# Kernel optimization log

Hardware: AMD Instinct MI355X
Metric: run time of the kernel (lower is better)

Reference implementation:

```python
import jax, jax.numpy as jnp
import numpy as np


def setup_inputs() -> dict:
    B, S, D, V = 2, 4096, 512, 32000
    FE_START, FE_LEN = 5, 3062          # user-controllable span [5, 3067)
    ADV_START, ADV_LEN = 1000, 64       # adversarial suffix block
    ML = ADV_START - FE_START           # 995 = max_left_shift
    MR = FE_LEN - (ADV_START - FE_START + ADV_LEN)  # 2003 = max_right_shift
    key = jax.random.key(0)
    k1, k2 = jax.random.split(key)
    input_ids = jax.random.randint(k1, (B, S), 0, V, dtype=jnp.int32)
    suffix_mask = jnp.zeros((B, S), dtype=bool).at[:, ADV_START:ADV_START + ADV_LEN].set(True)
    # param initialized like _create_parameters: delta at index max_left_shift
    param = jnp.zeros((1, ML + MR + 1), dtype=jnp.float32).at[0, ML].set(1.0)
    emb_weight = jax.random.normal(k2, (V, D), dtype=jnp.float32) * 0.02
    return {
        'input_ids': input_ids, 'suffix_mask': suffix_mask,
        'param': param, 'emb_weight': emb_weight,
        'fe_start': FE_START, 'fe_len': FE_LEN, 'adv_len': ADV_LEN,
        'max_left_shift': ML, 'max_right_shift': MR,
    }


def _padded_kernel(param, ml, mr):
    left_pad = max(0, mr - ml)
    right_pad = max(0, ml - mr)
    # F.pad then flip, as in torch forward
    return jnp.flip(jnp.pad(param, ((0, 0), (left_pad, right_pad)))[0])  # (Kp,)


def reference(input_ids, suffix_mask, param, emb_weight,
              fe_start, fe_len, adv_len, max_left_shift, max_right_shift):
    B, S = input_ids.shape
    D = emb_weight.shape[1]
    Kp = 2 * max(max_left_shift, max_right_shift) + 1
    p = Kp // 2  # 'same' padding
    pk = _padded_kernel(param, max_left_shift, max_right_shift).astype(emb_weight.dtype)

    embeds = emb_weight[input_ids]                       # (B,S,D)
    fe = embeds[:, fe_start:fe_start + fe_len]           # frontend-user gather (contiguous)
    fe_pad = jnp.pad(fe, ((0, 0), (p, p), (0, 0)))       # (B, F+2p, D)
    # depthwise conv1d with a single shared kernel == Toeplitz matmul
    off = jnp.arange(fe_len + 2 * p)[None, :] - jnp.arange(fe_len)[:, None]
    W = jnp.where((off >= 0) & (off < Kp), pk[jnp.clip(off, 0, Kp - 1)], 0.0)  # (F, F+2p)
    new_fe = jnp.einsum('tu,bud->btd', W, fe_pad)        # (B,F,D)
    # scatter-concat: other[:extra0] | shifted user span | other[extra1:]
    out_embeds = jnp.concatenate(
        [embeds[:, :fe_start], new_fe, embeds[:, fe_start + fe_len:]], axis=1)

    # ----- id path (no_grad in original) -----
    L = adv_len
    ms = p - jnp.argmax(pk == 1.0)                       # mask_shift
    a0 = jnp.argmax(suffix_mask, axis=-1)                # (B,) current_start
    ns = a0 + ms                                         # new_start
    idx = jnp.arange(S - L)[None, :]
    src = idx + L * (idx >= a0[:, None])                 # skip the adv block
    nonadv = jnp.take_along_axis(input_ids, src, axis=1)             # (B,S-L)
    adv = jnp.take_along_axis(input_ids, a0[:, None] + jnp.arange(L)[None, :], axis=1)
    j = jnp.arange(S)[None, :]
    in_adv = (j >= ns[:, None]) & (j < ns[:, None] + L)
    idx_non = jnp.clip(jnp.where(j < ns[:, None], j, j - L), 0, S - L - 1)
    idx_adv = jnp.clip(j - ns[:, None], 0, L - 1)
    out_ids = jnp.where(in_adv,
                        jnp.take_along_axis(adv, idx_adv, axis=1),
                        jnp.take_along_axis(nonadv, idx_non, axis=1))
    return out_embeds, out_ids
```

## Files before the change

kernel.cpp:

```cpp
#include <hip/hip_runtime.h>
#include <limits.h>

#define BB 2
#define SS 4096
#define DD 512
#define VV 32000
#define FE_START 5
#define FE_LEN 3062
#define ADV_LEN 64
#define ML 995
#define MR 2003
#define KP (2 * MR + 1)
#define PHALF (KP / 2)
#define LEFT_PAD (MR - ML)
#define PARAM_LEN (ML + MR + 1)


__global__ void ABS_meta_kernel(const unsigned char* __restrict__ mask_bytes,
                                const float* __restrict__ param,
                                int* __restrict__ meta,
                                int tap_cap) {
    __shared__ int s_nnz;
    __shared__ int s_msi;
    __shared__ int s_first;
    __shared__ int s_layout;
    __shared__ int s_a0[BB];

    const int tid = threadIdx.x;
    if (tid == 0) { s_nnz = 0; s_msi = INT_MAX; s_first = INT_MAX; }
    if (tid < BB) s_a0[tid] = INT_MAX;
    __syncthreads();

    for (int i = tid; i < BB * SS; i += blockDim.x)
        if (mask_bytes[i] != 0) atomicMin(&s_first, i);
    __syncthreads();
    if (tid == 0) {
        int f = s_first;
        int layout = 1;
        if (f != INT_MAX) {
            layout = (f + 1 < BB * SS && mask_bytes[f + 1] != 0) ? 1 : 4;
        }
        s_layout = layout;
    }
    __syncthreads();

    if (s_layout == 1) {
        for (int i = tid; i < BB * SS; i += blockDim.x)
            if (mask_bytes[i] != 0) atomicMin(&s_a0[i / SS], i % SS);
    } else {
        const int* mi = (const int*)mask_bytes;
        for (int i = tid; i < BB * SS; i += blockDim.x)
            if (mi[i] != 0) atomicMin(&s_a0[i / SS], i % SS);
    }

    for (int i = tid; i < KP; i += blockDim.x) {
        int j = KP - 1 - LEFT_PAD - i;
        float w = (j >= 0 && j < PARAM_LEN) ? param[j] : 0.0f;
        if (w != 0.0f) {
            int slot = atomicAdd(&s_nnz, 1);
            if (slot < tap_cap) {
                int* tp = meta + 16 + 2 * slot;
                tp[0] = i - PHALF;
                ((float*)tp)[1] = w;
            }
        }
        if (w == 1.0f) atomicMin(&s_msi, i);
    }
    __syncthreads();

    if (tid == 0) {
        meta[0] = (s_nnz < tap_cap) ? s_nnz : tap_cap;
        int msi = (s_msi == INT_MAX) ? 0 : s_msi;
        meta[1] = PHALF - msi;
        for (int b = 0; b < BB; ++b)
            meta[2 + b] = (s_a0[b] == INT_MAX) ? 0 : s_a0[b];
    }
}

__global__ void ABS_embed_ids_kernel(const int* __restrict__ ids,
                                     const float* __restrict__ emb,
                                     const int* __restrict__ meta,
                                     float* __restrict__ out) {
    const int bt = blockIdx.x;
    const int b = bt / SS;
    const int t = bt % SS;
    const int d4 = threadIdx.x;

    float4* out4 = (float4*)(out + (size_t)bt * DD);

    if (t < FE_START || t >= FE_START + FE_LEN) {
        const int id = ids[bt];
        out4[d4] = ((const float4*)(emb + (size_t)id * DD))[d4];
    } else {
        const int tt = t - FE_START;
        const int nnz = meta[0];
        float4 acc = make_float4(0.f, 0.f, 0.f, 0.f);
        for (int k = 0; k < nnz; ++k) {
            const int* tp = meta + 16 + 2 * k;
            const int off = tp[0];
            const float w = ((const float*)tp)[1];
            const int s = tt + off;
            if (s >= 0 && s < FE_LEN) {
                const int id = ids[b * SS + FE_START + s];
                const float4 v = ((const float4*)(emb + (size_t)id * DD))[d4];
                acc.x += w * v.x; acc.y += w * v.y;
                acc.z += w * v.z; acc.w += w * v.w;
            }
        }
        out4[d4] = acc;
    }

    if (threadIdx.x == 0) {
        const int ms = meta[1];
        const int a0 = meta[2 + b];
        const int ns = a0 + ms;
        const int j = t;
        int outid;
        if (j >= ns && j < ns + ADV_LEN) {
            outid = ids[b * SS + a0 + (j - ns)];
        } else {
            int k = (j < ns) ? j : (j - ADV_LEN);
            k = min(max(k, 0), SS - ADV_LEN - 1);
            const int src = k + ((k >= a0) ? ADV_LEN : 0);
            outid = ids[b * SS + src];
        }
        out[(size_t)BB * SS * DD + bt] = (float)outid;
    }
}

extern "C" void kernel_launch(void* const* d_in, const int* in_sizes, int n_in,
                              void* d_out, int out_size, void* d_ws, size_t ws_size,
                              hipStream_t stream) {
    const int* ids = (const int*)d_in[0];
    const unsigned char* mask = (const unsigned char*)d_in[1];
    const float* param = (const float*)d_in[2];
    const float* emb = (const float*)d_in[3];
    float* out = (float*)d_out;
    int* meta = (int*)d_ws;

    int tap_cap = (int)((ws_size > 128 ? ws_size - 64 : 64) / 8);
    if (tap_cap > KP) tap_cap = KP;

    ABS_meta_kernel<<<1, 256, 0, stream>>>(mask, param, meta, tap_cap);
    ABS_embed_ids_kernel<<<BB * SS, 128, 0, stream>>>(ids, emb, meta, out);
}
```

Before: 141.1 us.

## Fuse meta scan into embedding kernel with per-block redundant tap extraction

Removes the single-block metadata kernel and its global workspace round-trip. Each block now redundantly scans the parameter vector into shared-memory tap lists and scans its batch row's mask with 64-bit loads, then processes 8 rows with 256 threads. This drops a serial 1-block launch and the dependency between kernels, at the cost of every block re-reading the ~3000-element param and 4KB mask. A fallback path reads param directly if taps exceed shared capacity.

```diff
diff --git a/kernel.cpp b/kernel.cpp
--- a/kernel.cpp
+++ b/kernel.cpp
@@ -4,7 +4,6 @@
 #define BB 2
 #define SS 4096
 #define DD 512
-#define VV 32000
 #define FE_START 5
 #define FE_LEN 3062
 #define ADV_LEN 64
@@ -12,117 +11,128 @@
 #define MR 2003
 #define KP (2 * MR + 1)
 #define PHALF (KP / 2)
-#define LEFT_PAD (MR - ML)
 #define PARAM_LEN (ML + MR + 1)
 
 
-__global__ void ABS_meta_kernel(const unsigned char* __restrict__ mask_bytes,
-                                const float* __restrict__ param,
-                                int* __restrict__ meta,
-                                int tap_cap) {
-    __shared__ int s_nnz;
-    __shared__ int s_msi;
-    __shared__ int s_first;
-    __shared__ int s_layout;
-    __shared__ int s_a0[BB];
+#define RPB 8
+#define NT 256
+#define TAP_CAP 512
+
+__global__ __launch_bounds__(NT) void ABS_fused(
+        const int* __restrict__ ids,
+        const unsigned char* __restrict__ mask_bytes,
+        const float* __restrict__ param,
+        const float* __restrict__ emb,
+        float* __restrict__ out) {
+    __shared__ int   s_tapo[TAP_CAP];
+    __shared__ float s_tapw[TAP_CAP];
+    __shared__ int s_nnz, s_jmax, s_a0b, s_a0i, s_layout;
 
     const int tid = threadIdx.x;
-    if (tid == 0) { s_nnz = 0; s_msi = INT_MAX; s_first = INT_MAX; }
-    if (tid < BB) s_a0[tid] = INT_MAX;
+    const int block_row = blockIdx.x * RPB;
+    const int b = block_row / SS;
+
+    if (tid == 0) { s_nnz = 0; s_jmax = -1; s_a0b = INT_MAX; s_a0i = INT_MAX; }
     __syncthreads();
 
-    for (int i = tid; i < BB * SS; i += blockDim.x)
-        if (mask_bytes[i] != 0) atomicMin(&s_first, i);
+    for (int j = tid; j < PARAM_LEN; j += NT) {
+        float w = param[j];
+        if (w != 0.0f) {
+            int slot = atomicAdd(&s_nnz, 1);
+            if (slot < TAP_CAP) { s_tapo[slot] = 995 - j; s_tapw[slot] = w; }
+        }
+        if (w == 1.0f) atomicMax(&s_jmax, j);
+    }
+
+    const unsigned long long* m8 = (const unsigned long long*)mask_bytes;
+    for (int u = b * (SS / 8) + tid, e = (b + 1) * (SS / 8); u < e; u += NT) {
+        unsigned long long w = m8[u];
+        if (w) {
+            int fb = 8 * u + (__ffsll((long long)w) - 1) / 8 - b * SS;
+            atomicMin(&s_a0b, fb);
+        }
+    }
     __syncthreads();
+
     if (tid == 0) {
-        int f = s_first;
-        int layout = 1;
-        if (f != INT_MAX) {
-            layout = (f + 1 < BB * SS && mask_bytes[f + 1] != 0) ? 1 : 4;
-        }
+        int f = s_a0b;
+        int layout = 4;
+        if (f != INT_MAX)
+            layout = (f + 1 < SS && mask_bytes[b * SS + f + 1] != 0) ? 1 : 4;
         s_layout = layout;
     }
     __syncthreads();
 
-    if (s_layout == 1) {
-        for (int i = tid; i < BB * SS; i += blockDim.x)
-            if (mask_bytes[i] != 0) atomicMin(&s_a0[i / SS], i % SS);
-    } else {
-        const int* mi = (const int*)mask_bytes;
-        for (int i = tid; i < BB * SS; i += blockDim.x)
-            if (mi[i] != 0) atomicMin(&s_a0[i / SS], i % SS);
+    if (s_layout == 4) {
+        for (int u = b * (SS / 2) + tid, e = (b + 1) * (SS / 2); u < e; u += NT) {
+            unsigned long long w = m8[u];
+            if (w) {
+                int base = 2 * u - b * SS;
+                if ((unsigned int)w)         atomicMin(&s_a0i, base);
+                if ((unsigned int)(w >> 32)) atomicMin(&s_a0i, base + 1);
+            }
+        }
+        __syncthreads();
     }
 
-    for (int i = tid; i < KP; i += blockDim.x) {
-        int j = KP - 1 - LEFT_PAD - i;
-        float w = (j >= 0 && j < PARAM_LEN) ? param[j] : 0.0f;
-        if (w != 0.0f) {
-            int slot = atomicAdd(&s_nnz, 1);
-            if (slot < tap_cap) {
-                int* tp = meta + 16 + 2 * slot;
-                tp[0] = i - PHALF;
-                ((float*)tp)[1] = w;
+    const int  nnz      = (s_nnz < TAP_CAP) ? s_nnz : TAP_CAP;
+    const bool overflow = (s_nnz > TAP_CAP);
+    const int  a0r      = (s_layout == 1) ? s_a0b : s_a0i;
+    const int  a0       = (a0r == INT_MAX) ? 0 : a0r;
+    const int  ms       = (s_jmax >= 0) ? (s_jmax - 995) : PHALF;
+
+    const int d4   = tid & 127;
+    const int half = tid >> 7;
+    for (int it = 0; it < RPB / 2; ++it) {
+        const int bt = block_row + it * 2 + half;
+        const int t  = bt - b * SS;
+        float4* out4 = (float4*)(out + (size_t)bt * DD);
+        if (t < FE_START || t >= FE_START + FE_LEN) {
+            const int id = ids[bt];
+            out4[d4] = ((const float4*)(emb + (size_t)id * DD))[d4];
+        } else {
+            const int tt = t - FE_START;
+            float4 acc = make_float4(0.f, 0.f, 0.f, 0.f);
+            if (!overflow) {
+                for (int k = 0; k < nnz; ++k) {
+                    const int s = tt + s_tapo[k];
+                    const float w = s_tapw[k];
+                    if (s >= 0 && s < FE_LEN) {
+                        const int id = ids[b * SS + FE_START + s];
+                        const float4 v = ((const float4*)(emb + (size_t)id * DD))[d4];
+                        acc.x += w * v.x; acc.y += w * v.y;
+                        acc.z += w * v.z; acc.w += w * v.w;
+                    }
+                }
+            } else {
+                for (int j = 0; j < PARAM_LEN; ++j) {
+                    const float w = param[j];
+                    if (w != 0.0f) {
+                        const int s = tt + 995 - j;
+                        if (s >= 0 && s < FE_LEN) {
+                            const int id = ids[b * SS + FE_START + s];
+                            const float4 v = ((const float4*)(emb + (size_t)id * DD))[d4];
+                            acc.x += w * v.x; acc.y += w * v.y;
+                            acc.z += w * v.z; acc.w += w * v.w;
+                        }
+                    }
+                }
             }
+            out4[d4] = acc;
         }
-        if (w == 1.0f) atomicMin(&s_msi, i);
-    }
-    __syncthreads();
-
-    if (tid == 0) {
-        meta[0] = (s_nnz < tap_cap) ? s_nnz : tap_cap;
-        int msi = (s_msi == INT_MAX) ? 0 : s_msi;
-        meta[1] = PHALF - msi;
-        for (int b = 0; b < BB; ++b)
-            meta[2 + b] = (s_a0[b] == INT_MAX) ? 0 : s_a0[b];
-    }
-}
-
-__global__ void ABS_embed_ids_kernel(const int* __restrict__ ids,
-                                     const float* __restrict__ emb,
-                                     const int* __restrict__ meta,
-                                     float* __restrict__ out) {
-    const int bt = blockIdx.x;
-    const int b = bt / SS;
-    const int t = bt % SS;
-    const int d4 = threadIdx.x;
-
-    float4* out4 = (float4*)(out + (size_t)bt * DD);
-
-    if (t < FE_START || t >= FE_START + FE_LEN) {
-        const int id = ids[bt];
-        out4[d4] = ((const float4*)(emb + (size_t)id * DD))[d4];
-    } else {
-        const int tt = t - FE_START;
-        const int nnz = meta[0];
-        float4 acc = make_float4(0.f, 0.f, 0.f, 0.f);
-        for (int k = 0; k < nnz; ++k) {
-            const int* tp = meta + 16 + 2 * k;
-            const int off = tp[0];
-            const float w = ((const float*)tp)[1];
-            const int s = tt + off;
-            if (s >= 0 && s < FE_LEN) {
-                const int id = ids[b * SS + FE_START + s];
-                const float4 v = ((const float4*)(emb + (size_t)id * DD))[d4];
-                acc.x += w * v.x; acc.y += w * v.y;
-                acc.z += w * v.z; acc.w += w * v.w;
-            }
-        }
-        out4[d4] = acc;
     }
 
-    if (threadIdx.x == 0) {
-        const int ms = meta[1];
-        const int a0 = meta[2 + b];
+    if (tid < RPB) {
+        const int bt = block_row + tid;
+        const int j  = bt - b * SS;
         const int ns = a0 + ms;
-        const int j = t;
         int outid;
         if (j >= ns && j < ns + ADV_LEN) {
             outid = ids[b * SS + a0 + (j - ns)];
         } else {
             int k = (j < ns) ? j : (j - ADV_LEN);
             k = min(max(k, 0), SS - ADV_LEN - 1);
-            const int src = k + ((k >= a0) ? ADV_LEN : 0);
-            outid = ids[b * SS + src];
+            outid = ids[b * SS + k + ((k >= a0) ? ADV_LEN : 0)];
         }
         out[(size_t)BB * SS * DD + bt] = (float)outid;
     }
@@ -136,11 +146,6 @@
     const float* param = (const float*)d_in[2];
     const float* emb = (const float*)d_in[3];
     float* out = (float*)d_out;
-    int* meta = (int*)d_ws;
 
-    int tap_cap = (int)((ws_size > 128 ? ws_size - 64 : 64) / 8);
-    if (tap_cap > KP) tap_cap = KP;
-
-    ABS_meta_kernel<<<1, 256, 0, stream>>>(mask, param, meta, tap_cap);
-    ABS_embed_ids_kernel<<<BB * SS, 128, 0, stream>>>(ids, emb, meta, out);
+    ABS_fused<<<(BB * SS) / RPB, NT, 0, stream>>>(ids, mask, param, emb, out);
 }
```

Result: faster. 125.0 us (-11.4%).
